# Kernel optimization log

Measured on AMD Instinct MI355X. Metric: run time of the kernel, lower is better.

## Reference

```python
import jax, jax.numpy as jnp
import numpy as np

E, D, A = 1024, 1024, 512

def setup_inputs() -> dict:
    key = jax.random.key(0)
    ks = jax.random.split(key, 8)
    B, S = 32, 2048
    s_e = 1.0 / np.sqrt(E)
    s_d = 1.0 / np.sqrt(D)
    s_a = 1.0 / np.sqrt(A)
    return {
        "encoder_outputs": jax.random.normal(ks[0], (B, S, E), jnp.float32),
        "decoder_hidden": jax.random.normal(ks[1], (B, D), jnp.float32),
        "We": jax.random.uniform(ks[2], (E, A), jnp.float32, -s_e, s_e),
        "be": jax.random.uniform(ks[3], (A,), jnp.float32, -s_e, s_e),
        "Wd": jax.random.uniform(ks[4], (D, A), jnp.float32, -s_d, s_d),
        "bd": jax.random.uniform(ks[5], (A,), jnp.float32, -s_d, s_d),
        "v_w": jax.random.uniform(ks[6], (A,), jnp.float32, -s_a, s_a),
        "v_b": jax.random.uniform(ks[7], (), jnp.float32, -s_a, s_a),
    }

def reference(encoder_outputs, decoder_hidden, We, be, Wd, bd, v_w, v_b):
    # encoder_energy: [B,S,A]; decoder_energy: [B,1,A]
    enc_e = jnp.einsum('bse,ea->bsa', encoder_outputs, We) + be
    dec_e = (decoder_hidden @ Wd + bd)[:, None, :]
    energy = jnp.tanh(enc_e + dec_e)                     # [B,S,A]
    scores = jnp.einsum('bsa,a->bs', energy, v_w) + v_b  # [B,S]
    attn = jax.nn.softmax(scores, axis=1)                # [B,S]
    context = jnp.einsum('bs,bse->be', attn, encoder_outputs)  # [B,E]
    return context, attn
```

## Files before the change

kernel.cpp:

```cpp
#include <hip/hip_runtime.h>
#include <math.h>

#define E_DIM 1024
#define D_DIM 1024
#define A_DIM 512
#define B_NUM 32
#define S_DIM 2048
#define M_DIM (B_NUM * S_DIM)

typedef unsigned short ushort;
typedef short short8 __attribute__((ext_vector_type(8)));
typedef float f32x4 __attribute__((ext_vector_type(4)));
typedef unsigned short ushort4v __attribute__((ext_vector_type(4)));

typedef const void __attribute__((address_space(1))) cglobal_t;
typedef void __attribute__((address_space(3))) lds_t;

__device__ __forceinline__ void gload_lds16(const void* g, void* l) {
    __builtin_amdgcn_global_load_lds((cglobal_t*)g, (lds_t*)l, 16, 0, 0);
}

__device__ __forceinline__ ushort f2bf(float x) {
    unsigned u = __float_as_uint(x);
    u += 0x7FFF + ((u >> 16) & 1);
    return (ushort)(u >> 16);
}

__device__ __forceinline__ unsigned cvt_pk_bf16(float lo, float hi) {
    unsigned r;
    asm("v_cvt_pk_bf16_f32 %0, %1, %2" : "=v"(r) : "v"(lo), "v"(hi));
    return r;
}

__device__ __forceinline__ float bf2f(unsigned hi16_in_low) {
    return __uint_as_float(hi16_in_low << 16);
}

__device__ __forceinline__ float fast_tanh(float x) {
    const float e = __expf(2.0f * x);
    return 1.0f - 2.0f * __builtin_amdgcn_rcpf(e + 1.0f);
}

__global__ __launch_bounds__(256) void k0c_cvt_enc(
    const float* __restrict__ enc, ushort* __restrict__ ebf) {
    const size_t stride = (size_t)gridDim.x * 256;
    const size_t n8 = (size_t)M_DIM * E_DIM / 8;
    for (size_t i = (size_t)blockIdx.x * 256 + threadIdx.x; i < n8; i += stride) {
        const float4 a = *reinterpret_cast<const float4*>(enc + i * 8);
        const float4 b = *reinterpret_cast<const float4*>(enc + i * 8 + 4);
        *reinterpret_cast<int4*>(ebf + i * 8) =
            make_int4(cvt_pk_bf16(a.x, a.y), cvt_pk_bf16(a.z, a.w),
                      cvt_pk_bf16(b.x, b.y), cvt_pk_bf16(b.z, b.w));
    }
}

__global__ __launch_bounds__(256) void k0_dec_energy(
    const float* __restrict__ dh, const float* __restrict__ Wd,
    const float* __restrict__ bd, const float* __restrict__ be,
    float* __restrict__ dec2) {
    __shared__ float sdh[D_DIM];
    const int b = blockIdx.y;
    const int t = threadIdx.x;
    for (int i = t; i < D_DIM; i += 256) sdh[i] = dh[b * D_DIM + i];
    __syncthreads();
    const int a = blockIdx.x * 256 + t;
    float acc = bd[a] + be[a];
#pragma unroll 8
    for (int e = 0; e < D_DIM; ++e) acc += sdh[e] * Wd[(size_t)e * A_DIM + a];
    dec2[b * A_DIM + a] = acc;
}

__global__ __launch_bounds__(256) void k0b_cvt_we(
    const float* __restrict__ We, ushort* __restrict__ Wt) {
    const int n = blockIdx.x;
    const int k0 = threadIdx.x * 4;
    ushort4v v;
#pragma unroll
    for (int j = 0; j < 4; ++j) v[j] = f2bf(We[(size_t)(k0 + j) * A_DIM + n]);
    *reinterpret_cast<ushort4v*>(&Wt[(size_t)n * E_DIM + k0]) = v;
}

#define BM 128
#define BN 128
#define BK 32

__global__ __launch_bounds__(256, 3) void k1_mfma_gload(
    const ushort* __restrict__ ebf, const ushort* __restrict__ Wt,
    const float* __restrict__ dec2, const float* __restrict__ v_w,
    float* __restrict__ pscores) {
    __shared__ ushort As[BM * BK];
    __shared__ ushort Bs[BN * BK];

    const int t = threadIdx.x;
    const int l = t & 63;
    const int w = t >> 6;
    const int wm = w >> 1, wn = w & 1;
    const int fr = l & 15;
    const int kg = l >> 4;

    const int o = ((blockIdx.x & 7) << 8) | (blockIdx.x >> 3);
    const int x = o >> 2, y = o & 3;
    const int row0 = x * BM;
    const int n0 = y * BN;
    const int b = row0 >> 11;

    const ushort* Ag = ebf + (size_t)(row0 + w * 32 + (l >> 2)) * E_DIM + (l & 3) * 8;
    const ushort* Bg = Wt + (size_t)(n0 + w * 32 + (l >> 2)) * E_DIM + (l & 3) * 8;
    ushort* Al = As + w * 1024;
    ushort* Bl = Bs + w * 1024;

    f32x4 acc[4][4];
#pragma unroll
    for (int i = 0; i < 4; ++i)
#pragma unroll
        for (int j = 0; j < 4; ++j) acc[i][j] = (f32x4){0.f, 0.f, 0.f, 0.f};

    for (int kt = 0; kt < E_DIM / BK; ++kt) {
        const int koff = kt * BK;
        gload_lds16(Ag + koff, Al);
        gload_lds16(Ag + 16 * E_DIM + koff, Al + 512);
        gload_lds16(Bg + koff, Bl);
        gload_lds16(Bg + 16 * E_DIM + koff, Bl + 512);
        __syncthreads();

        short8 af[4], bf[4];
#pragma unroll
        for (int i = 0; i < 4; ++i)
            af[i] = *reinterpret_cast<const short8*>(As + (wm * 64 + i * 16 + fr) * 32 + kg * 8);
#pragma unroll
        for (int j = 0; j < 4; ++j)
            bf[j] = *reinterpret_cast<const short8*>(Bs + (wn * 64 + j * 16 + fr) * 32 + kg * 8);
#pragma unroll
        for (int i = 0; i < 4; ++i)
#pragma unroll
            for (int j = 0; j < 4; ++j)
                acc[i][j] = __builtin_amdgcn_mfma_f32_16x16x32_bf16(af[i], bf[j], acc[i][j], 0, 0, 0);
        __syncthreads();
    }

    float rowsum[4][4];
#pragma unroll
    for (int i = 0; i < 4; ++i)
#pragma unroll
        for (int r = 0; r < 4; ++r) rowsum[i][r] = 0.0f;

#pragma unroll
    for (int j = 0; j < 4; ++j) {
        const int ag = n0 + wn * 64 + j * 16 + fr;
        const float bias = dec2[b * A_DIM + ag];
        const float vw = v_w[ag];
#pragma unroll
        for (int i = 0; i < 4; ++i)
#pragma unroll
            for (int r = 0; r < 4; ++r)
                rowsum[i][r] += fast_tanh(acc[i][j][r] + bias) * vw;
    }
#pragma unroll
    for (int m = 1; m < 16; m <<= 1)
#pragma unroll
        for (int i = 0; i < 4; ++i)
#pragma unroll
            for (int r = 0; r < 4; ++r)
                rowsum[i][r] += __shfl_xor(rowsum[i][r], m, 64);

    __syncthreads();
    float* red = reinterpret_cast<float*>(As);
    if (fr == 0) {
#pragma unroll
        for (int i = 0; i < 4; ++i)
#pragma unroll
            for (int r = 0; r < 4; ++r)
                red[(wm * 64 + i * 16 + kg * 4 + r) * 2 + wn] = rowsum[i][r];
    }
    __syncthreads();
    if (t < BM)
        pscores[(size_t)(row0 + t) * 4 + y] = red[t * 2] + red[t * 2 + 1];
}

#define PAD 40
__global__ __launch_bounds__(256, 2) void k1_mfma_reg(
    const float* __restrict__ enc, const ushort* __restrict__ Wt,
    const float* __restrict__ dec2, const float* __restrict__ v_w,
    float* __restrict__ pscores) {
    __shared__ ushort As[2][BM][PAD];
    __shared__ ushort Bs[2][BN][PAD];

    const int t = threadIdx.x;
    const int l = t & 63;
    const int w = t >> 6;
    const int wm = w >> 1, wn = w & 1;
    const int fr = l & 15;
    const int kg = l >> 4;

    const int o = ((blockIdx.x & 7) << 8) | (blockIdx.x >> 3);
    const int x = o >> 2, y = o & 3;
    const int row0 = x * BM;
    const int n0 = y * BN;
    const int b = row0 >> 11;

    const int srow = t >> 1;
    const int skh = (t & 1) * 16;

    const float* Ag = enc + (size_t)(row0 + srow) * E_DIM + skh;
    const ushort* Bg = Wt + (size_t)(n0 + srow) * E_DIM + skh;

    f32x4 acc[4][4];
#pragma unroll
    for (int i = 0; i < 4; ++i)
#pragma unroll
        for (int j = 0; j < 4; ++j) acc[i][j] = (f32x4){0.f, 0.f, 0.f, 0.f};

    float4 pa[4];
    int4 pb[2];

#define STAGE_LOAD(k0)                                              \
    {                                                               \
        pa[0] = *reinterpret_cast<const float4*>(Ag + (k0));        \
        pa[1] = *reinterpret_cast<const float4*>(Ag + (k0) + 4);    \
        pa[2] = *reinterpret_cast<const float4*>(Ag + (k0) + 8);    \
        pa[3] = *reinterpret_cast<const float4*>(Ag + (k0) + 12);   \
        pb[0] = *reinterpret_cast<const int4*>(Bg + (k0));          \
        pb[1] = *reinterpret_cast<const int4*>(Bg + (k0) + 8);      \
    }

#define STAGE_WRITE(buf)                                                  \
    {                                                                     \
        unsigned uu[8];                                                   \
        _Pragma("unroll") for (int q = 0; q < 4; ++q) {                   \
            uu[2 * q] = cvt_pk_bf16(pa[q].x, pa[q].y);                    \
            uu[2 * q + 1] = cvt_pk_bf16(pa[q].z, pa[q].w);                \
        }                                                                 \
        *reinterpret_cast<int4*>(&As[buf][srow][skh]) =                   \
            make_int4(uu[0], uu[1], uu[2], uu[3]);                        \
        *reinterpret_cast<int4*>(&As[buf][srow][skh + 8]) =               \
            make_int4(uu[4], uu[5], uu[6], uu[7]);                        \
        *reinterpret_cast<int4*>(&Bs[buf][srow][skh]) = pb[0];            \
        *reinterpret_cast<int4*>(&Bs[buf][srow][skh + 8]) = pb[1];        \
    }

    STAGE_LOAD(0);
    STAGE_WRITE(0);
    __syncthreads();

    for (int kt = 0; kt < E_DIM / BK; ++kt) {
        const int cur = kt & 1;
        if (kt < E_DIM / BK - 1) STAGE_LOAD((kt + 1) * BK);

        short8 af[4], bf[4];
#pragma unroll
        for (int i = 0; i < 4; ++i)
            af[i] = *reinterpret_cast<const short8*>(&As[cur][wm * 64 + i * 16 + fr][kg * 8]);
#pragma unroll
        for (int j = 0; j < 4; ++j)
            bf[j] = *reinterpret_cast<const short8*>(&Bs[cur][wn * 64 + j * 16 + fr][kg * 8]);
#pragma unroll
        for (int i = 0; i < 4; ++i)
#pragma unroll
            for (int j = 0; j < 4; ++j)
                acc[i][j] = __builtin_amdgcn_mfma_f32_16x16x32_bf16(af[i], bf[j], acc[i][j], 0, 0, 0);

        if (kt < E_DIM / BK - 1) STAGE_WRITE(cur ^ 1);
        __syncthreads();
    }

    float rowsum[4][4];
#pragma unroll
    for (int i = 0; i < 4; ++i)
#pragma unroll
        for (int r = 0; r < 4; ++r) rowsum[i][r] = 0.0f;
#pragma unroll
    for (int j = 0; j < 4; ++j) {
        const int ag = n0 + wn * 64 + j * 16 + fr;
        const float bias = dec2[b * A_DIM + ag];
        const float vw = v_w[ag];
#pragma unroll
        for (int i = 0; i < 4; ++i)
#pragma unroll
            for (int r = 0; r < 4; ++r)
                rowsum[i][r] += fast_tanh(acc[i][j][r] + bias) * vw;
    }
#pragma unroll
    for (int m = 1; m < 16; m <<= 1)
#pragma unroll
        for (int i = 0; i < 4; ++i)
#pragma unroll
            for (int r = 0; r < 4; ++r)
                rowsum[i][r] += __shfl_xor(rowsum[i][r], m, 64);

    __syncthreads();
    float* red = reinterpret_cast<float*>(&As[0][0][0]);
    if (fr == 0) {
#pragma unroll
        for (int i = 0; i < 4; ++i)
#pragma unroll
            for (int r = 0; r < 4; ++r)
                red[(wm * 64 + i * 16 + kg * 4 + r) * 2 + wn] = rowsum[i][r];
    }
    __syncthreads();
    if (t < BM)
        pscores[(size_t)(row0 + t) * 4 + y] = red[t * 2] + red[t * 2 + 1];
}

__global__ __launch_bounds__(256) void k2_softmax(
    const float* __restrict__ pscores, const float* __restrict__ v_b,
    float* __restrict__ attn_out) {
    __shared__ float sc[S_DIM];
    __shared__ float red[8];
    const int b = blockIdx.x;
    const int t = threadIdx.x;
    const int wave = t >> 6, lane = t & 63;
    const float vb = v_b[0];

    float lmax = -1e30f;
    for (int s = t; s < S_DIM; s += 256) {
        const float4 p = *reinterpret_cast<const float4*>(&pscores[(size_t)(b * S_DIM + s) * 4]);
        const float v = p.x + p.y + p.z + p.w + vb;
        sc[s] = v;
        lmax = fmaxf(lmax, v);
    }
#pragma unroll
    for (int off = 32; off > 0; off >>= 1) lmax = fmaxf(lmax, __shfl_down(lmax, off, 64));
    if (lane == 0) red[wave] = lmax;
    __syncthreads();
    const float bmax = fmaxf(fmaxf(red[0], red[1]), fmaxf(red[2], red[3]));

    float lsum = 0.0f;
    for (int s = t; s < S_DIM; s += 256) {
        const float e = expf(sc[s] - bmax);
        sc[s] = e;
        lsum += e;
    }
#pragma unroll
    for (int off = 32; off > 0; off >>= 1) lsum += __shfl_down(lsum, off, 64);
    if (lane == 0) red[4 + wave] = lsum;
    __syncthreads();
    const float inv = 1.0f / (red[4] + red[5] + red[6] + red[7]);
    for (int s = t; s < S_DIM; s += 256) attn_out[b * S_DIM + s] = sc[s] * inv;
}

#define SC_CHUNK 128
#define N_SC (S_DIM / SC_CHUNK)
__global__ __launch_bounds__(128) void k3_ctx_bf16(
    const ushort* __restrict__ ebf, const float* __restrict__ attn,
    float* __restrict__ pctx) {
    const int b = blockIdx.y;
    const int scb = blockIdx.x;
    const int t = threadIdx.x;
    const int s0 = scb * SC_CHUNK;
    float acc[8];
#pragma unroll
    for (int j = 0; j < 8; ++j) acc[j] = 0.0f;
    const ushort* base = ebf + (size_t)(b * S_DIM + s0) * E_DIM + t * 8;
#pragma unroll 4
    for (int s = 0; s < SC_CHUNK; ++s) {
        const float wgt = attn[b * S_DIM + s0 + s];
        const int4 v = *reinterpret_cast<const int4*>(base + (size_t)s * E_DIM);
        const unsigned* u = reinterpret_cast<const unsigned*>(&v);
#pragma unroll
        for (int j = 0; j < 4; ++j) {
            acc[2 * j] += wgt * __uint_as_float(u[j] << 16);
            acc[2 * j + 1] += wgt * __uint_as_float(u[j] & 0xffff0000u);
        }
    }
    float* dst = &pctx[(size_t)(b * N_SC + scb) * E_DIM + t * 8];
    *reinterpret_cast<float4*>(dst) = make_float4(acc[0], acc[1], acc[2], acc[3]);
    *reinterpret_cast<float4*>(dst + 4) = make_float4(acc[4], acc[5], acc[6], acc[7]);
}

__global__ __launch_bounds__(256) void k3_ctx_partial(
    const float* __restrict__ enc, const float* __restrict__ attn,
    float* __restrict__ pctx) {
    const int b = blockIdx.y;
    const int scb = blockIdx.x;
    const int t = threadIdx.x;
    const int s0 = scb * SC_CHUNK;
    float4 acc = {0.0f, 0.0f, 0.0f, 0.0f};
    const float4* encv =
        reinterpret_cast<const float4*>(enc + (size_t)(b * S_DIM + s0) * E_DIM);
#pragma unroll 4
    for (int s = 0; s < SC_CHUNK; ++s) {
        const float w = attn[b * S_DIM + s0 + s];
        const float4 v = encv[(size_t)s * (E_DIM / 4) + t];
        acc.x += w * v.x;
        acc.y += w * v.y;
        acc.z += w * v.z;
        acc.w += w * v.w;
    }
    *reinterpret_cast<float4*>(&pctx[(size_t)(b * N_SC + scb) * E_DIM + t * 4]) = acc;
}

__global__ __launch_bounds__(256) void k4_ctx_reduce(
    const float* __restrict__ pctx, float* __restrict__ ctx) {
    const int b = blockIdx.x;
    const int t = threadIdx.x;
    float4 acc = {0.0f, 0.0f, 0.0f, 0.0f};
#pragma unroll
    for (int s = 0; s < N_SC; ++s) {
        const float4 v = *reinterpret_cast<const float4*>(
            &pctx[(size_t)(b * N_SC + s) * E_DIM + t * 4]);
        acc.x += v.x;
        acc.y += v.y;
        acc.z += v.z;
        acc.w += v.w;
    }
    *reinterpret_cast<float4*>(&ctx[(size_t)b * E_DIM + t * 4]) = acc;
}

extern "C" void kernel_launch(void* const* d_in, const int* in_sizes, int n_in,
                              void* d_out, int out_size, void* d_ws, size_t ws_size,
                              hipStream_t stream) {
    (void)in_sizes; (void)n_in; (void)out_size;
    const float* enc = (const float*)d_in[0];
    const float* dh  = (const float*)d_in[1];
    const float* We  = (const float*)d_in[2];
    const float* be  = (const float*)d_in[3];
    const float* Wd  = (const float*)d_in[4];
    const float* bd  = (const float*)d_in[5];
    const float* vw  = (const float*)d_in[6];
    const float* vb  = (const float*)d_in[7];

    float* out = (float*)d_out;
    float* ctx_out = out;
    float* attn_out = out + B_NUM * E_DIM;

    const size_t NEED = 138477568ULL;

    if (ws_size >= NEED) {
        char* W = (char*)d_ws;
        ushort* ebf    = (ushort*)W;
        ushort* Wt     = (ushort*)(W + 134217728);
        float* dec2    = (float*)(W + 135266304);
        float* pscores = (float*)(W + 135331840);
        float* pctx    = (float*)(W + 136380416);

        k0c_cvt_enc<<<dim3(2048), 256, 0, stream>>>(enc, ebf);
        k0_dec_energy<<<dim3(2, 32), 256, 0, stream>>>(dh, Wd, bd, be, dec2);
        k0b_cvt_we<<<dim3(A_DIM), 256, 0, stream>>>(We, Wt);
        k1_mfma_gload<<<dim3((M_DIM / BM) * (A_DIM / BN)), 256, 0, stream>>>(
            ebf, Wt, dec2, vw, pscores);
        k2_softmax<<<dim3(B_NUM), 256, 0, stream>>>(pscores, vb, attn_out);
        k3_ctx_bf16<<<dim3(N_SC, B_NUM), 128, 0, stream>>>(ebf, attn_out, pctx);
        k4_ctx_reduce<<<dim3(B_NUM), 256, 0, stream>>>(pctx, ctx_out);
    } else {
        float* ws = (float*)d_ws;
        float* dec2    = ws;
        float* pscores = ws + 16384;
        float* pctx    = ws + 16384 + 262144;
        ushort* Wt     = (ushort*)(ws + 16384 + 262144 + 524288);

        k0_dec_energy<<<dim3(2, 32), 256, 0, stream>>>(dh, Wd, bd, be, dec2);
        k0b_cvt_we<<<dim3(A_DIM), 256, 0, stream>>>(We, Wt);
        k1_mfma_reg<<<dim3((M_DIM / BM) * (A_DIM / BN)), 256, 0, stream>>>(
            enc, Wt, dec2, vw, pscores);
        k2_softmax<<<dim3(B_NUM), 256, 0, stream>>>(pscores, vb, attn_out);
        k3_ctx_partial<<<dim3(N_SC, B_NUM), 256, 0, stream>>>(enc, attn_out, pctx);
        k4_ctx_reduce<<<dim3(B_NUM), 256, 0, stream>>>(pctx, ctx_out);
    }
}
```

Baseline: 257.9 us.

## Replace GEMM-score kernel with 256x256 8-wave triple-buffered LDS pipeline

After: 244.9 us. 1.05x faster.

```diff
diff --git a/kernel.cpp b/kernel.cpp
--- a/kernel.cpp
+++ b/kernel.cpp
@@ -30,10 +30,6 @@
     unsigned r;
     asm("v_cvt_pk_bf16_f32 %0, %1, %2" : "=v"(r) : "v"(lo), "v"(hi));
     return r;
-}
-
-__device__ __forceinline__ float bf2f(unsigned hi16_in_low) {
-    return __uint_as_float(hi16_in_low << 16);
 }
 
 __device__ __forceinline__ float fast_tanh(float x) {
@@ -80,67 +76,107 @@
     *reinterpret_cast<ushort4v*>(&Wt[(size_t)n * E_DIM + k0]) = v;
 }
 
-#define BM 128
-#define BN 128
-#define BK 32
-
-__global__ __launch_bounds__(256, 3) void k1_mfma_gload(
+#define BM2 256
+#define BN2 256
+#define BK2 32
+#define NT2 (E_DIM / BK2)
+#define BUFU 16384
+
+__global__ __launch_bounds__(512, 2) void k1_mfma_8w(
     const ushort* __restrict__ ebf, const ushort* __restrict__ Wt,
     const float* __restrict__ dec2, const float* __restrict__ v_w,
     float* __restrict__ pscores) {
-    __shared__ ushort As[BM * BK];
-    __shared__ ushort Bs[BN * BK];
+    __shared__ ushort L[3 * BUFU];
 
     const int t = threadIdx.x;
     const int l = t & 63;
     const int w = t >> 6;
-    const int wm = w >> 1, wn = w & 1;
+    const int wm = w >> 2;
+    const int wn = w & 3;
     const int fr = l & 15;
     const int kg = l >> 4;
 
-    const int o = ((blockIdx.x & 7) << 8) | (blockIdx.x >> 3);
-    const int x = o >> 2, y = o & 3;
-    const int row0 = x * BM;
-    const int n0 = y * BN;
+    const int o = ((blockIdx.x & 7) << 6) | (blockIdx.x >> 3);
+    const int x = o >> 1, ny = o & 1;
+    const int row0 = x * BM2;
+    const int n0 = ny * BN2;
     const int b = row0 >> 11;
 
-    const ushort* Ag = ebf + (size_t)(row0 + w * 32 + (l >> 2)) * E_DIM + (l & 3) * 8;
-    const ushort* Bg = Wt + (size_t)(n0 + w * 32 + (l >> 2)) * E_DIM + (l & 3) * 8;
-    ushort* Al = As + w * 1024;
-    ushort* Bl = Bs + w * 1024;
-
-    f32x4 acc[4][4];
-#pragma unroll
-    for (int i = 0; i < 4; ++i)
+    const int sA0 = t, sA1 = 512 + t;
+    const int rA0 = sA0 >> 2, rA1 = sA1 >> 2;
+    const int cA0 = (sA0 & 3) ^ ((rA0 >> 1) & 3);
+    const int cA1 = (sA1 & 3) ^ ((rA1 >> 1) & 3);
+    const ushort* srcA0 = ebf + (size_t)(row0 + rA0) * E_DIM + cA0 * 8;
+    const ushort* srcA1 = ebf + (size_t)(row0 + rA1) * E_DIM + cA1 * 8;
+    const ushort* srcB0 = Wt + (size_t)(n0 + rA0) * E_DIM + cA0 * 8;
+    const ushort* srcB1 = Wt + (size_t)(n0 + rA1) * E_DIM + cA1 * 8;
+    const int ldsA0 = w * 512;
+    const int ldsA1 = 4096 + w * 512;
+    const int ldsB0 = 8192 + w * 512;
+    const int ldsB1 = 8192 + 4096 + w * 512;
+
+#define STAGE2(cb, kt)                                             \
+    {                                                              \
+        const int ko = (kt) * BK2;                                 \
+        ushort* base = L + (cb) * BUFU;                            \
+        gload_lds16(srcA0 + ko, base + ldsA0);                     \
+        gload_lds16(srcA1 + ko, base + ldsA1);                     \
+        gload_lds16(srcB0 + ko, base + ldsB0);                     \
+        gload_lds16(srcB1 + ko, base + ldsB1);                     \
+    }
+
+    f32x4 acc[8][4];
+#pragma unroll
+    for (int i = 0; i < 8; ++i)
 #pragma unroll
         for (int j = 0; j < 4; ++j) acc[i][j] = (f32x4){0.f, 0.f, 0.f, 0.f};
 
-    for (int kt = 0; kt < E_DIM / BK; ++kt) {
-        const int koff = kt * BK;
-        gload_lds16(Ag + koff, Al);
-        gload_lds16(Ag + 16 * E_DIM + koff, Al + 512);
-        gload_lds16(Bg + koff, Bl);
-        gload_lds16(Bg + 16 * E_DIM + koff, Bl + 512);
-        __syncthreads();
-
-        short8 af[4], bf[4];
-#pragma unroll
-        for (int i = 0; i < 4; ++i)
-            af[i] = *reinterpret_cast<const short8*>(As + (wm * 64 + i * 16 + fr) * 32 + kg * 8);
-#pragma unroll
-        for (int j = 0; j < 4; ++j)
-            bf[j] = *reinterpret_cast<const short8*>(Bs + (wn * 64 + j * 16 + fr) * 32 + kg * 8);
-#pragma unroll
-        for (int i = 0; i < 4; ++i)
+    STAGE2(0, 0);
+    STAGE2(1, 1);
+    asm volatile("s_waitcnt vmcnt(4)" ::: "memory");
+    __builtin_amdgcn_s_barrier();
+
+    int cbuf = 0, pbuf = 2;
+    for (int kt = 0; kt < NT2; ++kt) {
+        if (kt < NT2 - 2) STAGE2(pbuf, kt + 2);
+
+        const ushort* Ab = L + cbuf * BUFU;
+        const ushort* Bb = Ab + 8192;
+        short8 af[8], bf[4];
+#pragma unroll
+        for (int i = 0; i < 8; ++i) {
+            const int r = wm * 128 + i * 16 + fr;
+            af[i] = *reinterpret_cast<const short8*>(
+                Ab + r * 32 + ((kg ^ ((r >> 1) & 3)) << 3));
+        }
+#pragma unroll
+        for (int j = 0; j < 4; ++j) {
+            const int r = wn * 64 + j * 16 + fr;
+            bf[j] = *reinterpret_cast<const short8*>(
+                Bb + r * 32 + ((kg ^ ((r >> 1) & 3)) << 3));
+        }
+        __builtin_amdgcn_s_setprio(1);
+#pragma unroll
+        for (int i = 0; i < 8; ++i)
 #pragma unroll
             for (int j = 0; j < 4; ++j)
                 acc[i][j] = __builtin_amdgcn_mfma_f32_16x16x32_bf16(af[i], bf[j], acc[i][j], 0, 0, 0);
-        __syncthreads();
-    }
-
-    float rowsum[4][4];
-#pragma unroll
-    for (int i = 0; i < 4; ++i)
+        __builtin_amdgcn_s_setprio(0);
+
+        if (kt < NT2 - 2) {
+            asm volatile("s_waitcnt vmcnt(4)" ::: "memory");
+        } else if (kt == NT2 - 2) {
+            asm volatile("s_waitcnt vmcnt(0)" ::: "memory");
+        }
+        __builtin_amdgcn_s_barrier();
+
+        cbuf = (cbuf == 2) ? 0 : cbuf + 1;
+        pbuf = (pbuf == 2) ? 0 : pbuf + 1;
+    }
+
+    float rowsum[8][4];
+#pragma unroll
+    for (int i = 0; i < 8; ++i)
 #pragma unroll
         for (int r = 0; r < 4; ++r) rowsum[i][r] = 0.0f;
 
@@ -150,7 +186,7 @@
         const float bias = dec2[b * A_DIM + ag];
         const float vw = v_w[ag];
 #pragma unroll
-        for (int i = 0; i < 4; ++i)
+        for (int i = 0; i < 8; ++i)
 #pragma unroll
             for (int r = 0; r < 4; ++r)
                 rowsum[i][r] += fast_tanh(acc[i][j][r] + bias) * vw;
@@ -158,25 +194,29 @@
 #pragma unroll
     for (int m = 1; m < 16; m <<= 1)
 #pragma unroll
-        for (int i = 0; i < 4; ++i)
+        for (int i = 0; i < 8; ++i)
 #pragma unroll
             for (int r = 0; r < 4; ++r)
                 rowsum[i][r] += __shfl_xor(rowsum[i][r], m, 64);
 
-    __syncthreads();
-    float* red = reinterpret_cast<float*>(As);
+    float* red = reinterpret_cast<float*>(L);
     if (fr == 0) {
 #pragma unroll
-        for (int i = 0; i < 4; ++i)
-#pragma unroll
-            for (int r = 0; r < 4; ++r)
-                red[(wm * 64 + i * 16 + kg * 4 + r) * 2 + wn] = rowsum[i][r];
-    }
-    __syncthreads();
-    if (t < BM)
-        pscores[(size_t)(row0 + t) * 4 + y] = red[t * 2] + red[t * 2 + 1];
-}
-
+        for (int i = 0; i < 8; ++i)
+#pragma unroll
+            for (int r = 0; r < 4; ++r)
+                red[(wm * 128 + i * 16 + kg * 4 + r) * 4 + wn] = rowsum[i][r];
+    }
+    __syncthreads();
+    if (t < BM2) {
+        const float s = red[t * 4] + red[t * 4 + 1] + red[t * 4 + 2] + red[t * 4 + 3];
+        pscores[(size_t)(row0 + t) * 2 + ny] = s;
+    }
+}
+
+#define BM 128
+#define BN 128
+#define BK 32
 #define PAD 40
 __global__ __launch_bounds__(256, 2) void k1_mfma_reg(
     const float* __restrict__ enc, const ushort* __restrict__ Wt,
@@ -303,7 +343,7 @@
 
 __global__ __launch_bounds__(256) void k2_softmax(
     const float* __restrict__ pscores, const float* __restrict__ v_b,
-    float* __restrict__ attn_out) {
+    float* __restrict__ attn_out, int W) {
     __shared__ float sc[S_DIM];
     __shared__ float red[8];
     const int b = blockIdx.x;
@@ -313,8 +353,8 @@
 
     float lmax = -1e30f;
     for (int s = t; s < S_DIM; s += 256) {
-        const float4 p = *reinterpret_cast<const float4*>(&pscores[(size_t)(b * S_DIM + s) * 4]);
-        const float v = p.x + p.y + p.z + p.w + vb;
+        float v = vb;
+        for (int c = 0; c < W; ++c) v += pscores[(size_t)(b * S_DIM + s) * W + c];
         sc[s] = v;
         lmax = fmaxf(lmax, v);
     }
@@ -436,9 +476,9 @@
         k0c_cvt_enc<<<dim3(2048), 256, 0, stream>>>(enc, ebf);
         k0_dec_energy<<<dim3(2, 32), 256, 0, stream>>>(dh, Wd, bd, be, dec2);
         k0b_cvt_we<<<dim3(A_DIM), 256, 0, stream>>>(We, Wt);
-        k1_mfma_gload<<<dim3((M_DIM / BM) * (A_DIM / BN)), 256, 0, stream>>>(
+        k1_mfma_8w<<<dim3((M_DIM / BM2) * (A_DIM / BN2)), 512, 0, stream>>>(
             ebf, Wt, dec2, vw, pscores);
-        k2_softmax<<<dim3(B_NUM), 256, 0, stream>>>(pscores, vb, attn_out);
+        k2_softmax<<<dim3(B_NUM), 256, 0, stream>>>(pscores, vb, attn_out, 2);
         k3_ctx_bf16<<<dim3(N_SC, B_NUM), 128, 0, stream>>>(ebf, attn_out, pctx);
         k4_ctx_reduce<<<dim3(B_NUM), 256, 0, stream>>>(pctx, ctx_out);
     } else {
@@ -452,7 +492,7 @@
         k0b_cvt_we<<<dim3(A_DIM), 256, 0, stream>>>(We, Wt);
         k1_mfma_reg<<<dim3((M_DIM / BM) * (A_DIM / BN)), 256, 0, stream>>>(
             enc, Wt, dec2, vw, pscores);
-        k2_softmax<<<dim3(B_NUM), 256, 0, stream>>>(pscores, vb, attn_out);
+        k2_softmax<<<dim3(B_NUM), 256, 0, stream>>>(pscores, vb, attn_out, 4);
         k3_ctx_partial<<<dim3(N_SC, B_NUM), 256, 0, stream>>>(enc, attn_out, pctx);
         k4_ctx_reduce<<<dim3(B_NUM), 256, 0, stream>>>(pctx, ctx_out);
     }
```
